# Performance work log

Measured on AMD Instinct MI355X. Metric: run time of the kernel, lower is better.

The kernel has to match this reference:

```python
import jax, jax.numpy as jnp
import numpy as np

N_NODES = 50000
N_EDGES = 800000
F_IN = 128
HID = 256


def setup_inputs() -> dict:
    key = jax.random.key(0)
    ks = jax.random.split(key, 10)
    x = jax.random.normal(ks[0], (N_NODES, F_IN), jnp.float32)
    edge_index = jax.random.randint(ks[1], (2, N_EDGES), 0, N_NODES, jnp.int32)
    # Glorot-ish scaled weights (PyG Linear default init style)
    def w(k, o, i):
        return jax.random.normal(k, (o, i), jnp.float32) * (1.0 / np.sqrt(i))
    return {
        "x": x,
        "edge_index": edge_index,
        "W1l": w(ks[2], HID, F_IN), "b1l": jnp.zeros((HID,), jnp.float32),
        "W1r": w(ks[3], HID, F_IN),
        "W2l": w(ks[4], HID, HID), "b2l": jnp.zeros((HID,), jnp.float32),
        "W2r": w(ks[5], HID, HID),
        "Wh1": w(ks[6], 4, HID), "bh1": jnp.zeros((4,), jnp.float32),
        "Wh2": w(ks[7], 3, HID), "bh2": jnp.zeros((3,), jnp.float32),
    }


def sage_conv(x, edge_index, Wl, bl, Wr):
    # PyG SAGEConv (aggr='mean'): out_i = Wl @ mean_{j in N(i)} x_j + bl + Wr @ x_i
    src, dst = edge_index[0], edge_index[1]
    n = x.shape[0]
    summed = jax.ops.segment_sum(x[src], dst, num_segments=n)        # [N, F]
    cnt = jax.ops.segment_sum(jnp.ones((src.shape[0],), x.dtype), dst, num_segments=n)
    agg = summed / jnp.maximum(cnt, 1.0)[:, None]                    # isolated nodes -> 0
    return agg @ Wl.T + bl + x @ Wr.T


def reference(x, edge_index, W1l, b1l, W1r, W2l, b2l, W2r, Wh1, bh1, Wh2, bh2):
    h = jax.nn.relu(sage_conv(x, edge_index, W1l, b1l, W1r))
    # dropout(p=0.5) is identity in eval mode
    h = sage_conv(h, edge_index, W2l, b2l, W2r)
    out1 = h @ Wh1.T + bh1   # l2_classifier=False branch
    out2 = h @ Wh2.T + bh2
    return (out1, out2, h)
```

## Files before the change

kernel.cpp:

```cpp
#include <hip/hip_runtime.h>
#include <hip/hip_bf16.h>

typedef short bf16x8 __attribute__((ext_vector_type(8)));
typedef float f32x4 __attribute__((ext_vector_type(4)));

__device__ __forceinline__ float bf2f(__hip_bfloat16 v) { return __bfloat162float(v); }
__device__ __forceinline__ float sh2f(short s) {
    union { float f; unsigned u; } c; c.u = ((unsigned)(unsigned short)s) << 16; return c.f;
}
__device__ __forceinline__ short f2sh(float f) {
    __hip_bfloat16 b = __float2bfloat16(f); return *(short*)&b;
}

__device__ __forceinline__ float loadAny(const void* p, size_t i, int isf32) {
    return isf32 ? ((const float*)p)[i] : bf2f(((const __hip_bfloat16*)p)[i]);
}

__global__ void pre_kernel(const void* __restrict__ x,
                           const void* W1l, const void* W1r, const void* W2l, const void* W2r,
                           const void* b1l, const void* b2l, const void* Wh1, const void* Wh2,
                           const void* bh1, const void* bh2,
                           __hip_bfloat16* __restrict__ xn,
                           __hip_bfloat16* __restrict__ W1c, __hip_bfloat16* __restrict__ W2c,
                           __hip_bfloat16* __restrict__ sb,
                           int* __restrict__ deg, int* __restrict__ flag, int N) {
    __shared__ int sflag;
    int tid = threadIdx.x;
    if (tid < 64) {
        const unsigned short* xu = (const unsigned short*)x;
        unsigned short u = xu[tid * 2];
        unsigned e = (u >> 7) & 0xFF;
        bool good = (u == 0) || (e >= 110 && e <= 137);
        unsigned long long m = __ballot(good);
        if (tid == 0) sflag = (__popcll(m) < 32) ? 1 : 0;
    }
    __syncthreads();
    int isf32 = sflag;
    int gid = blockIdx.x * 256 + tid;
    if (gid == 0) *flag = isf32;
    if (gid < N) deg[gid] = 0;

    int n4 = N * 32;
    if (gid < n4) {
        short4 o;
        if (isf32) {
            float4 v = ((const float4*)x)[gid];
            o.x = f2sh(v.x); o.y = f2sh(v.y); o.z = f2sh(v.z); o.w = f2sh(v.w);
        } else {
            o = ((const short4*)x)[gid];
        }
        ((short4*)xn)[gid] = o;
    }

    if (gid < 65536) {
        int n = gid >> 8, k = gid & 255;
        float v = (k < 128) ? loadAny(W1l, n * 128 + k, isf32)
                            : loadAny(W1r, n * 128 + (k - 128), isf32);
        W1c[gid] = __float2bfloat16(v);
        return;
    }
    int u = gid - 65536;
    if (u < 131072) {
        int n = u >> 9, k = u & 511;
        float v = (k < 256) ? loadAny(W2l, n * 256 + k, isf32)
                            : loadAny(W2r, n * 256 + (k - 256), isf32);
        W2c[u] = __float2bfloat16(v);
        return;
    }
    int s = u - 131072;
    float v;
    if      (s < 256)  v = loadAny(b1l, s, isf32);
    else if (s < 512)  v = loadAny(b2l, s - 256, isf32);
    else if (s < 1536) v = loadAny(Wh1, s - 512, isf32);
    else if (s < 2304) v = loadAny(Wh2, s - 1536, isf32);
    else if (s < 2308) v = loadAny(bh1, s - 2304, isf32);
    else if (s < 2311) v = loadAny(bh2, s - 2308, isf32);
    else return;
    sb[s] = __float2bfloat16(v);
}

__global__ void deg_kernel(const int* __restrict__ ei, int E, int* __restrict__ deg,
                           int* __restrict__ rank) {
    int t = blockIdx.x * blockDim.x + threadIdx.x;
    if (t >= E) return;
    rank[t] = atomicAdd(&deg[ei[E + t]], 1);
}

__global__ __launch_bounds__(256) void scanA_kernel(const int* __restrict__ deg,
                                                    int* __restrict__ off,
                                                    int* __restrict__ bsum, int N) {
    __shared__ int ts[256];
    int t = threadIdx.x;
    int base = blockIdx.x * 1024 + t * 4;
    int v0 = (base + 0 < N) ? deg[base + 0] : 0;
    int v1 = (base + 1 < N) ? deg[base + 1] : 0;
    int v2 = (base + 2 < N) ? deg[base + 2] : 0;
    int v3 = (base + 3 < N) ? deg[base + 3] : 0;
    int i0 = v0, i1 = i0 + v1, i2 = i1 + v2, i3 = i2 + v3;
    ts[t] = i3;
    __syncthreads();
    for (int d = 1; d < 256; d <<= 1) {
        int x = (t >= d) ? ts[t - d] : 0;
        __syncthreads();
        ts[t] += x;
        __syncthreads();
    }
    int excl = (t > 0) ? ts[t - 1] : 0;
    if (base + 0 < N) off[base + 1] = excl + i0;
    if (base + 1 < N) off[base + 2] = excl + i1;
    if (base + 2 < N) off[base + 3] = excl + i2;
    if (base + 3 < N) off[base + 4] = excl + i3;
    if (t == 255) bsum[blockIdx.x] = ts[255];
}

__global__ void addC_kernel(int* __restrict__ off, const int* __restrict__ bsum,
                            int N, int nb) {
    __shared__ int ex[64];
    int t = threadIdx.x;
    if (t < 64) {
        int v = (t < nb) ? bsum[t] : 0;
        for (int d = 1; d < 64; d <<= 1) {
            int y = __shfl_up(v, d, 64);
            if (t >= d) v += y;
        }
        ex[t] = v;
    }
    __syncthreads();
    int i = blockIdx.x * 256 + t;
    if (i == 0) off[0] = 0;
    if (i < N) {
        int b = i >> 10;
        int excl = (b > 0) ? ex[b - 1] : 0;
        off[i + 1] += excl;
    }
}

__global__ void fill_kernel(const int* __restrict__ ei, int E,
                            const int* __restrict__ off, const int* __restrict__ rank,
                            unsigned short* __restrict__ srcs) {
    int t = blockIdx.x * blockDim.x + threadIdx.x;
    if (t >= E) return;
    int dst = ei[E + t];
    int pos = off[dst] + rank[t];
    srcs[pos] = (unsigned short)ei[t];
}

__global__ void gather1_kernel(const __hip_bfloat16* __restrict__ x,
                               const int* __restrict__ off,
                               const unsigned short* __restrict__ srcs,
                               __hip_bfloat16* __restrict__ agg, int N) {
    int gid  = blockIdx.x * blockDim.x + threadIdx.x;
    int wid  = gid >> 6;
    int lane = threadIdx.x & 63;
    int node = wid * 4 + (lane >> 4);
    int t    = lane & 15;
    if (node >= N) return;
    int beg = off[node], end = off[node + 1];
    float a[8] = {0.f, 0.f, 0.f, 0.f, 0.f, 0.f, 0.f, 0.f};
    const bf16x8* xb = (const bf16x8*)x;
    int e = beg;
    for (; e + 7 < end; e += 8) {
        bf16x8 v[8];
#pragma unroll
        for (int j = 0; j < 8; j++) v[j] = xb[(size_t)srcs[e + j] * 16 + t];
#pragma unroll
        for (int j = 0; j < 8; j++)
#pragma unroll
            for (int k = 0; k < 8; k++) a[k] += sh2f(v[j][k]);
    }
    for (; e < end; e++) {
        bf16x8 v = xb[(size_t)srcs[e] * 16 + t];
#pragma unroll
        for (int k = 0; k < 8; k++) a[k] += sh2f(v[k]);
    }
    float inv = 1.0f / fmaxf((float)(end - beg), 1.0f);
    bf16x8 o;
#pragma unroll
    for (int k = 0; k < 8; k++) o[k] = f2sh(a[k] * inv);
    ((bf16x8*)agg)[(size_t)node * 16 + t] = o;
}

__global__ void gather2_kernel(const __hip_bfloat16* __restrict__ h,
                               const int* __restrict__ off,
                               const unsigned short* __restrict__ srcs,
                               __hip_bfloat16* __restrict__ agg, int N) {
    int gid  = blockIdx.x * blockDim.x + threadIdx.x;
    int wid  = gid >> 6;
    int lane = threadIdx.x & 63;
    int node = wid * 2 + (lane >> 5);
    int t    = lane & 31;
    if (node >= N) return;
    int beg = off[node], end = off[node + 1];
    float a[8] = {0.f, 0.f, 0.f, 0.f, 0.f, 0.f, 0.f, 0.f};
    const bf16x8* hb = (const bf16x8*)h;
    int e = beg;
    for (; e + 7 < end; e += 8) {
        bf16x8 v[8];
#pragma unroll
        for (int j = 0; j < 8; j++) v[j] = hb[(size_t)srcs[e + j] * 32 + t];
#pragma unroll
        for (int j = 0; j < 8; j++)
#pragma unroll
            for (int k = 0; k < 8; k++) a[k] += sh2f(v[j][k]);
    }
    for (; e < end; e++) {
        bf16x8 v = hb[(size_t)srcs[e] * 32 + t];
#pragma unroll
        for (int k = 0; k < 8; k++) a[k] += sh2f(v[k]);
    }
    float inv = 1.0f / fmaxf((float)(end - beg), 1.0f);
    bf16x8 o;
#pragma unroll
    for (int k = 0; k < 8; k++) o[k] = f2sh(a[k] * inv);
    ((bf16x8*)agg)[(size_t)node * 32 + t] = o;
}

template <int K, int KA, bool RELU, bool TOOUT>
__device__ __forceinline__ void gemm_body(short* wlds,
                                          const __hip_bfloat16* __restrict__ A1,
                                          const __hip_bfloat16* __restrict__ A2, int M,
                                          const __hip_bfloat16* __restrict__ W,
                                          const __hip_bfloat16* __restrict__ bias,
                                          __hip_bfloat16* __restrict__ outb,
                                          void* __restrict__ dout,
                                          const int* __restrict__ flag) {
    constexpr int KB = K - KA;
    constexpr int NCHUNK = K / 64;
    int rowBlks = (M + 63) / 64;
    int b = blockIdx.x;
    int grp = b >> 4, w = b & 15;
    int rowBlk = grp * 8 + (w & 7);
    int half = w >> 3;
    if (rowBlk >= rowBlks) return;
    int tid  = threadIdx.x;
    int wave = tid >> 6, lane = tid & 63, quad = lane >> 4, l15 = lane & 15;
    int R0 = rowBlk * 64;
    int cbase = half * 128;

    int mrow = min(R0 + wave * 16 + l15, M - 1);

    const short* Ws = (const short*)W;

    auto loadW = [&](int p, bf16x8* wreg) {
#pragma unroll
        for (int i = 0; i < 4; i++) {
            int unit = tid + i * 256;
            int ln = unit & 63, nt = (unit >> 6) & 7, kt = unit >> 9;
            int row = cbase + nt * 16 + (ln & 15);
            int kk  = p * 64 + kt * 32 + (ln >> 4) * 8;
            wreg[i] = *(const bf16x8*)(Ws + (size_t)row * K + kk);
        }
    };
    auto storeW = [&](const bf16x8* wreg) {
#pragma unroll
        for (int i = 0; i < 4; i++) {
            int unit = tid + i * 256;
            *(bf16x8*)&wlds[unit * 8] = wreg[i];
        }
    };
    auto loadA = [&](int kglob) {
        const short* ap = (kglob < KA)
            ? (const short*)A1 + (size_t)mrow * KA + kglob + quad * 8
            : (const short*)A2 + (size_t)mrow * KB + (kglob - KA) + quad * 8;
        return *(const bf16x8*)ap;
    };

    f32x4 acc[8];
#pragma unroll
    for (int nt = 0; nt < 8; nt++) acc[nt] = {0.f, 0.f, 0.f, 0.f};

    bf16x8 wreg[4];
    loadW(0, wreg);
    storeW(wreg);
    __syncthreads();
    bf16x8 a0f = loadA(0);
    bf16x8 a1f = loadA(32);

    for (int p = 0; p < NCHUNK; p++) {
        if (p + 1 < NCHUNK) loadW(p + 1, wreg);
#pragma unroll
        for (int kt = 0; kt < 2; kt++) {
            int kg = p * 64 + kt * 32;
            int kg2 = kg + 64;
            if (kg2 > K - 32) kg2 = K - 32;
            bf16x8 a_next = loadA(kg2);
#pragma unroll
            for (int nt = 0; nt < 8; nt++) {
                bf16x8 bfr = *(const bf16x8*)&wlds[((kt * 8 + nt) * 64 + lane) * 8];
                acc[nt] = __builtin_amdgcn_mfma_f32_16x16x32_bf16(a0f, bfr, acc[nt], 0, 0, 0);
            }
            a0f = a1f;
            a1f = a_next;
        }
        if (p + 1 < NCHUNK) {
            __syncthreads();
            storeW(wreg);
            __syncthreads();
        }
    }

    int isf32 = TOOUT ? *flag : 0;
    float* hf = TOOUT ? ((float*)dout + (size_t)M * 7) : nullptr;
    __hip_bfloat16* hb = TOOUT ? ((__hip_bfloat16*)dout + (size_t)M * 7) : outb;

#pragma unroll
    for (int nt = 0; nt < 8; nt++) {
        int col = cbase + nt * 16 + l15;
        float bv = bf2f(bias[col]);
#pragma unroll
        for (int r = 0; r < 4; r++) {
            int row = R0 + wave * 16 + quad * 4 + r;
            if (row < M) {
                float v = acc[nt][r] + bv;
                if (RELU) v = fmaxf(v, 0.f);
                size_t idx = (size_t)row * 256 + col;
                if (TOOUT && isf32) hf[idx] = v;
                else                hb[idx] = __float2bfloat16(v);
            }
        }
    }
}

__global__ __launch_bounds__(256) void gemm1_kernel(const __hip_bfloat16* __restrict__ A1,
                                                    const __hip_bfloat16* __restrict__ A2, int M,
                                                    const __hip_bfloat16* __restrict__ W,
                                                    const __hip_bfloat16* __restrict__ bias,
                                                    __hip_bfloat16* __restrict__ outb,
                                                    const int* __restrict__ flag) {
    __shared__ short wlds[8192];
    gemm_body<256, 128, true, false>(wlds, A1, A2, M, W, bias, outb, nullptr, flag);
}

__global__ __launch_bounds__(256) void gemm2_kernel(const __hip_bfloat16* __restrict__ A1,
                                                    const __hip_bfloat16* __restrict__ A2, int M,
                                                    const __hip_bfloat16* __restrict__ W,
                                                    const __hip_bfloat16* __restrict__ bias,
                                                    void* __restrict__ dout,
                                                    const int* __restrict__ flag) {
    __shared__ short wlds[8192];
    gemm_body<512, 256, false, true>(wlds, A1, A2, M, W, bias, nullptr, dout, flag);
}

__global__ void heads_kernel(const __hip_bfloat16* __restrict__ sb,
                             void* dout, int N, const int* __restrict__ flag) {
    int isf32 = *flag;
    int node = (blockIdx.x * blockDim.x + threadIdx.x) >> 6;
    int lane = threadIdx.x & 63;
    if (node >= N) return;
    float hv0, hv1, hv2, hv3;
    if (isf32) {
        const float4* hp = (const float4*)((const float*)dout + (size_t)N * 7);
        float4 v = hp[(size_t)node * 64 + lane];
        hv0 = v.x; hv1 = v.y; hv2 = v.z; hv3 = v.w;
    } else {
        const __hip_bfloat162* hp = (const __hip_bfloat162*)((const __hip_bfloat16*)dout + (size_t)N * 7);
        __hip_bfloat162 a = hp[(size_t)node * 128 + 2 * lane];
        __hip_bfloat162 b = hp[(size_t)node * 128 + 2 * lane + 1];
        hv0 = bf2f(a.x); hv1 = bf2f(a.y); hv2 = bf2f(b.x); hv3 = bf2f(b.y);
    }
#pragma unroll
    for (int r = 0; r < 7; r++) {
        const __hip_bfloat16* wrow = (r < 4) ? (sb + 512 + r * 256) : (sb + 1536 + (r - 4) * 256);
        const __hip_bfloat162* wr2 = (const __hip_bfloat162*)wrow;
        __hip_bfloat162 wa = wr2[2 * lane];
        __hip_bfloat162 wb = wr2[2 * lane + 1];
        float p = hv0 * bf2f(wa.x) + hv1 * bf2f(wa.y) + hv2 * bf2f(wb.x) + hv3 * bf2f(wb.y);
        for (int off = 32; off > 0; off >>= 1) p += __shfl_down(p, off, 64);
        if (lane == 0) {
            float bias = (r < 4) ? bf2f(sb[2304 + r]) : bf2f(sb[2308 + (r - 4)]);
            float v = p + bias;
            size_t idx = (r < 4) ? ((size_t)node * 4 + r)
                                 : ((size_t)N * 4 + (size_t)node * 3 + (r - 4));
            if (isf32) ((float*)dout)[idx] = v;
            else       ((__hip_bfloat16*)dout)[idx] = __float2bfloat16(v);
        }
    }
}

extern "C" void kernel_launch(void* const* d_in, const int* in_sizes, int n_in,
                              void* d_out, int out_size, void* d_ws, size_t ws_size,
                              hipStream_t stream) {
    const void* x   = d_in[0];
    const int*  ei  = (const int*)d_in[1];
    const void* W1l = d_in[2];
    const void* b1l = d_in[3];
    const void* W1r = d_in[4];
    const void* W2l = d_in[5];
    const void* b2l = d_in[6];
    const void* W2r = d_in[7];
    const void* Wh1 = d_in[8];
    const void* bh1 = d_in[9];
    const void* Wh2 = d_in[10];
    const void* bh2 = d_in[11];

    const int N = in_sizes[0] / 128;
    const int E = in_sizes[1] / 2;
    const int NB = (N + 1023) / 1024;

    char* ws = (char*)d_ws;
    int*            offp   = (int*)(ws + 0);
    int*            deg    = (int*)(ws + 262144);
    int*            bsum   = (int*)(ws + 524288);
    unsigned short* srcs   = (unsigned short*)(ws + 786432);
    __hip_bfloat16* W1c    = (__hip_bfloat16*)(ws + 3986432);
    __hip_bfloat16* W2c    = (__hip_bfloat16*)(ws + 4117504);
    __hip_bfloat16* sb     = (__hip_bfloat16*)(ws + 4379648);
    __hip_bfloat16* xn     = (__hip_bfloat16*)(ws + 4387840);
    __hip_bfloat16* h1     = (__hip_bfloat16*)(ws + 17187840);
    int*            rank   = (int*)(ws + 17187840);
    __hip_bfloat16* agg    = (__hip_bfloat16*)(ws + 42787840);
    int*            flag   = (int*)(ws + 68387840);

    pre_kernel<<<(N * 32 + 255) / 256, 256, 0, stream>>>(
        x, W1l, W1r, W2l, W2r, b1l, b2l, Wh1, Wh2, bh1, bh2,
        xn, W1c, W2c, sb, deg, flag, N);

    deg_kernel<<<(E + 255) / 256, 256, 0, stream>>>(ei, E, deg, rank);
    scanA_kernel<<<NB, 256, 0, stream>>>(deg, offp, bsum, N);
    addC_kernel<<<(N + 255) / 256, 256, 0, stream>>>(offp, bsum, N, NB);
    fill_kernel<<<(E + 255) / 256, 256, 0, stream>>>(ei, E, offp, rank, srcs);

    const int rowBlks = (N + 63) / 64;
    const int gemmGrid = ((rowBlks + 7) / 8) * 16;

    {
        int waves = (N + 3) / 4;
        gather1_kernel<<<(waves * 64 + 255) / 256, 256, 0, stream>>>(xn, offp, srcs, agg, N);
    }
    gemm1_kernel<<<gemmGrid, 256, 0, stream>>>(agg, xn, N, W1c, sb, h1, flag);

    {
        int waves = (N + 1) / 2;
        gather2_kernel<<<(waves * 64 + 255) / 256, 256, 0, stream>>>(h1, offp, srcs, agg, N);
    }
    gemm2_kernel<<<gemmGrid, 256, 0, stream>>>(agg, h1, N, W2c, sb + 256, d_out, flag);

    heads_kernel<<<(N + 3) / 4, 256, 0, stream>>>(sb, d_out, N, flag);
}
```

Baseline: 347.4 us.

## Fuse neighbor mean-gather into GEMM kernels with fragment-ordered weights

The separate gather kernels are removed. Each GEMM block now gathers and averages neighbor features for its 64 rows directly into swizzled LDS, then runs MFMA over the full 256 output columns. Weights are pre-permuted into MFMA fragment order so they can be read straight from global memory instead of being staged through LDS with syncs. This drops the agg round-trip through HBM and two kernel launches. In exchange, the gather's latency-bound loads now share blocks with the GEMM, the weight reads rely on cache reuse, and more accumulator registers are needed.

```diff
diff --git a/kernel.cpp b/kernel.cpp
--- a/kernel.cpp
+++ b/kernel.cpp
@@ -21,7 +21,7 @@
                            const void* b1l, const void* b2l, const void* Wh1, const void* Wh2,
                            const void* bh1, const void* bh2,
                            __hip_bfloat16* __restrict__ xn,
-                           __hip_bfloat16* __restrict__ W1c, __hip_bfloat16* __restrict__ W2c,
+                           __hip_bfloat16* __restrict__ W1f, __hip_bfloat16* __restrict__ W2f,
                            __hip_bfloat16* __restrict__ sb,
                            int* __restrict__ deg, int* __restrict__ flag, int N) {
     __shared__ int sflag;
@@ -56,7 +56,8 @@
         int n = gid >> 8, k = gid & 255;
         float v = (k < 128) ? loadAny(W1l, n * 128 + k, isf32)
                             : loadAny(W1r, n * 128 + (k - 128), isf32);
-        W1c[gid] = __float2bfloat16(v);
+        int idx = ((((k >> 5) * 16 + (n >> 4)) * 64) + ((k >> 3) & 3) * 16 + (n & 15)) * 8 + (k & 7);
+        W1f[idx] = __float2bfloat16(v);
         return;
     }
     int u = gid - 65536;
@@ -64,7 +65,8 @@
         int n = u >> 9, k = u & 511;
         float v = (k < 256) ? loadAny(W2l, n * 256 + k, isf32)
                             : loadAny(W2r, n * 256 + (k - 256), isf32);
-        W2c[u] = __float2bfloat16(v);
+        int idx = ((((k >> 5) * 16 + (n >> 4)) * 64) + ((k >> 3) & 3) * 16 + (n & 15)) * 8 + (k & 7);
+        W2f[idx] = __float2bfloat16(v);
         return;
     }
     int s = u - 131072;
@@ -145,158 +147,90 @@
     srcs[pos] = (unsigned short)ei[t];
 }
 
-__global__ void gather1_kernel(const __hip_bfloat16* __restrict__ x,
-                               const int* __restrict__ off,
-                               const unsigned short* __restrict__ srcs,
-                               __hip_bfloat16* __restrict__ agg, int N) {
-    int gid  = blockIdx.x * blockDim.x + threadIdx.x;
-    int wid  = gid >> 6;
-    int lane = threadIdx.x & 63;
-    int node = wid * 4 + (lane >> 4);
-    int t    = lane & 15;
-    if (node >= N) return;
-    int beg = off[node], end = off[node + 1];
-    float a[8] = {0.f, 0.f, 0.f, 0.f, 0.f, 0.f, 0.f, 0.f};
-    const bf16x8* xb = (const bf16x8*)x;
-    int e = beg;
-    for (; e + 7 < end; e += 8) {
-        bf16x8 v[8];
-#pragma unroll
-        for (int j = 0; j < 8; j++) v[j] = xb[(size_t)srcs[e + j] * 16 + t];
-#pragma unroll
-        for (int j = 0; j < 8; j++)
-#pragma unroll
-            for (int k = 0; k < 8; k++) a[k] += sh2f(v[j][k]);
-    }
-    for (; e < end; e++) {
-        bf16x8 v = xb[(size_t)srcs[e] * 16 + t];
-#pragma unroll
-        for (int k = 0; k < 8; k++) a[k] += sh2f(v[k]);
-    }
-    float inv = 1.0f / fmaxf((float)(end - beg), 1.0f);
-    bf16x8 o;
-#pragma unroll
-    for (int k = 0; k < 8; k++) o[k] = f2sh(a[k] * inv);
-    ((bf16x8*)agg)[(size_t)node * 16 + t] = o;
-}
-
-__global__ void gather2_kernel(const __hip_bfloat16* __restrict__ h,
-                               const int* __restrict__ off,
-                               const unsigned short* __restrict__ srcs,
-                               __hip_bfloat16* __restrict__ agg, int N) {
-    int gid  = blockIdx.x * blockDim.x + threadIdx.x;
-    int wid  = gid >> 6;
-    int lane = threadIdx.x & 63;
-    int node = wid * 2 + (lane >> 5);
-    int t    = lane & 31;
-    if (node >= N) return;
-    int beg = off[node], end = off[node + 1];
-    float a[8] = {0.f, 0.f, 0.f, 0.f, 0.f, 0.f, 0.f, 0.f};
-    const bf16x8* hb = (const bf16x8*)h;
-    int e = beg;
-    for (; e + 7 < end; e += 8) {
-        bf16x8 v[8];
-#pragma unroll
-        for (int j = 0; j < 8; j++) v[j] = hb[(size_t)srcs[e + j] * 32 + t];
-#pragma unroll
-        for (int j = 0; j < 8; j++)
-#pragma unroll
-            for (int k = 0; k < 8; k++) a[k] += sh2f(v[j][k]);
-    }
-    for (; e < end; e++) {
-        bf16x8 v = hb[(size_t)srcs[e] * 32 + t];
-#pragma unroll
-        for (int k = 0; k < 8; k++) a[k] += sh2f(v[k]);
-    }
-    float inv = 1.0f / fmaxf((float)(end - beg), 1.0f);
-    bf16x8 o;
-#pragma unroll
-    for (int k = 0; k < 8; k++) o[k] = f2sh(a[k] * inv);
-    ((bf16x8*)agg)[(size_t)node * 32 + t] = o;
-}
-
 template <int K, int KA, bool RELU, bool TOOUT>
-__device__ __forceinline__ void gemm_body(short* wlds,
-                                          const __hip_bfloat16* __restrict__ A1,
-                                          const __hip_bfloat16* __restrict__ A2, int M,
-                                          const __hip_bfloat16* __restrict__ W,
-                                          const __hip_bfloat16* __restrict__ bias,
-                                          __hip_bfloat16* __restrict__ outb,
-                                          void* __restrict__ dout,
-                                          const int* __restrict__ flag) {
-    constexpr int KB = K - KA;
-    constexpr int NCHUNK = K / 64;
-    int rowBlks = (M + 63) / 64;
-    int b = blockIdx.x;
-    int grp = b >> 4, w = b & 15;
-    int rowBlk = grp * 8 + (w & 7);
-    int half = w >> 3;
-    if (rowBlk >= rowBlks) return;
+__device__ __forceinline__ void gg_body(short* alds,
+                                        const __hip_bfloat16* __restrict__ T, int M,
+                                        const int* __restrict__ off,
+                                        const unsigned short* __restrict__ srcs,
+                                        const short* __restrict__ Wf,
+                                        const __hip_bfloat16* __restrict__ bias,
+                                        __hip_bfloat16* __restrict__ outb,
+                                        void* __restrict__ dout,
+                                        const int* __restrict__ flag) {
+    constexpr int UROW = KA / 8;
+    constexpr int LPN  = UROW;
+    constexpr int NPW  = 64 / LPN;
+    constexpr int ITER = 64 / (4 * NPW);
+    constexpr int KT   = K / 32;
+
     int tid  = threadIdx.x;
     int wave = tid >> 6, lane = tid & 63, quad = lane >> 4, l15 = lane & 15;
-    int R0 = rowBlk * 64;
-    int cbase = half * 128;
-
-    int mrow = min(R0 + wave * 16 + l15, M - 1);
-
-    const short* Ws = (const short*)W;
-
-    auto loadW = [&](int p, bf16x8* wreg) {
-#pragma unroll
-        for (int i = 0; i < 4; i++) {
-            int unit = tid + i * 256;
-            int ln = unit & 63, nt = (unit >> 6) & 7, kt = unit >> 9;
-            int row = cbase + nt * 16 + (ln & 15);
-            int kk  = p * 64 + kt * 32 + (ln >> 4) * 8;
-            wreg[i] = *(const bf16x8*)(Ws + (size_t)row * K + kk);
+    int R0 = blockIdx.x * 64;
+
+    {
+        int t    = lane & (LPN - 1);
+        int nsub = lane / LPN;
+        const bf16x8* tb = (const bf16x8*)T;
+#pragma unroll
+        for (int it = 0; it < ITER; ++it) {
+            int rloc = it * (4 * NPW) + wave * NPW + nsub;
+            int node = R0 + rloc;
+            if (node < M) {
+                int beg = off[node], end = off[node + 1];
+                float a[8] = {0.f, 0.f, 0.f, 0.f, 0.f, 0.f, 0.f, 0.f};
+                int e = beg;
+                for (; e + 7 < end; e += 8) {
+                    bf16x8 v[8];
+#pragma unroll
+                    for (int j = 0; j < 8; j++) v[j] = tb[(size_t)srcs[e + j] * UROW + t];
+#pragma unroll
+                    for (int j = 0; j < 8; j++)
+#pragma unroll
+                        for (int k = 0; k < 8; k++) a[k] += sh2f(v[j][k]);
+                }
+                for (; e < end; e++) {
+                    bf16x8 v = tb[(size_t)srcs[e] * UROW + t];
+#pragma unroll
+                    for (int k = 0; k < 8; k++) a[k] += sh2f(v[k]);
+                }
+                float inv = 1.0f / fmaxf((float)(end - beg), 1.0f);
+                bf16x8 o;
+#pragma unroll
+                for (int k = 0; k < 8; k++) o[k] = f2sh(a[k] * inv);
+                *(bf16x8*)&alds[(rloc * UROW + (t ^ (rloc & 7))) * 8] = o;
+            }
+        }
+    }
+    __syncthreads();
+
+    int rloc_m = wave * 16 + l15;
+    int mrow = min(R0 + rloc_m, M - 1);
+    const short* Ts = (const short*)T;
+
+    auto loadA = [&](int kglob) -> bf16x8 {
+        if (kglob < KA) {
+            int u = (kglob >> 3) + quad;
+            return *(const bf16x8*)&alds[(rloc_m * UROW + (u ^ (rloc_m & 7))) * 8];
+        } else {
+            return *(const bf16x8*)(Ts + (size_t)mrow * KA + (kglob - KA) + quad * 8);
         }
     };
-    auto storeW = [&](const bf16x8* wreg) {
-#pragma unroll
-        for (int i = 0; i < 4; i++) {
-            int unit = tid + i * 256;
-            *(bf16x8*)&wlds[unit * 8] = wreg[i];
-        }
-    };
-    auto loadA = [&](int kglob) {
-        const short* ap = (kglob < KA)
-            ? (const short*)A1 + (size_t)mrow * KA + kglob + quad * 8
-            : (const short*)A2 + (size_t)mrow * KB + (kglob - KA) + quad * 8;
-        return *(const bf16x8*)ap;
-    };
-
-    f32x4 acc[8];
-#pragma unroll
-    for (int nt = 0; nt < 8; nt++) acc[nt] = {0.f, 0.f, 0.f, 0.f};
-
-    bf16x8 wreg[4];
-    loadW(0, wreg);
-    storeW(wreg);
-    __syncthreads();
-    bf16x8 a0f = loadA(0);
-    bf16x8 a1f = loadA(32);
-
-    for (int p = 0; p < NCHUNK; p++) {
-        if (p + 1 < NCHUNK) loadW(p + 1, wreg);
-#pragma unroll
-        for (int kt = 0; kt < 2; kt++) {
-            int kg = p * 64 + kt * 32;
-            int kg2 = kg + 64;
-            if (kg2 > K - 32) kg2 = K - 32;
-            bf16x8 a_next = loadA(kg2);
-#pragma unroll
-            for (int nt = 0; nt < 8; nt++) {
-                bf16x8 bfr = *(const bf16x8*)&wlds[((kt * 8 + nt) * 64 + lane) * 8];
-                acc[nt] = __builtin_amdgcn_mfma_f32_16x16x32_bf16(a0f, bfr, acc[nt], 0, 0, 0);
-            }
-            a0f = a1f;
-            a1f = a_next;
-        }
-        if (p + 1 < NCHUNK) {
-            __syncthreads();
-            storeW(wreg);
-            __syncthreads();
-        }
+
+    f32x4 acc[16];
+#pragma unroll
+    for (int nt = 0; nt < 16; nt++) acc[nt] = {0.f, 0.f, 0.f, 0.f};
+
+    bf16x8 aCur = loadA(0);
+#pragma unroll
+    for (int kt = 0; kt < KT; ++kt) {
+        bf16x8 aNext = aCur;
+        if (kt + 1 < KT) aNext = loadA((kt + 1) * 32);
+#pragma unroll
+        for (int nt = 0; nt < 16; ++nt) {
+            bf16x8 b = *(const bf16x8*)(Wf + (size_t)((kt * 16 + nt) * 64 + lane) * 8);
+            acc[nt] = __builtin_amdgcn_mfma_f32_16x16x32_bf16(aCur, b, acc[nt], 0, 0, 0);
+        }
+        aCur = aNext;
     }
 
     int isf32 = TOOUT ? *flag : 0;
@@ -304,8 +238,8 @@
     __hip_bfloat16* hb = TOOUT ? ((__hip_bfloat16*)dout + (size_t)M * 7) : outb;
 
 #pragma unroll
-    for (int nt = 0; nt < 8; nt++) {
-        int col = cbase + nt * 16 + l15;
+    for (int nt = 0; nt < 16; nt++) {
+        int col = nt * 16 + l15;
         float bv = bf2f(bias[col]);
 #pragma unroll
         for (int r = 0; r < 4; r++) {
@@ -321,24 +255,28 @@
     }
 }
 
-__global__ __launch_bounds__(256) void gemm1_kernel(const __hip_bfloat16* __restrict__ A1,
-                                                    const __hip_bfloat16* __restrict__ A2, int M,
-                                                    const __hip_bfloat16* __restrict__ W,
-                                                    const __hip_bfloat16* __restrict__ bias,
-                                                    __hip_bfloat16* __restrict__ outb,
-                                                    const int* __restrict__ flag) {
-    __shared__ short wlds[8192];
-    gemm_body<256, 128, true, false>(wlds, A1, A2, M, W, bias, outb, nullptr, flag);
-}
-
-__global__ __launch_bounds__(256) void gemm2_kernel(const __hip_bfloat16* __restrict__ A1,
-                                                    const __hip_bfloat16* __restrict__ A2, int M,
-                                                    const __hip_bfloat16* __restrict__ W,
-                                                    const __hip_bfloat16* __restrict__ bias,
-                                                    void* __restrict__ dout,
-                                                    const int* __restrict__ flag) {
-    __shared__ short wlds[8192];
-    gemm_body<512, 256, false, true>(wlds, A1, A2, M, W, bias, nullptr, dout, flag);
+__global__ __launch_bounds__(256, 3) void gemm1_kernel(const __hip_bfloat16* __restrict__ xn,
+                                                       int M,
+                                                       const int* __restrict__ off,
+                                                       const unsigned short* __restrict__ srcs,
+                                                       const short* __restrict__ Wf,
+                                                       const __hip_bfloat16* __restrict__ bias,
+                                                       __hip_bfloat16* __restrict__ outb,
+                                                       const int* __restrict__ flag) {
+    __shared__ short alds[64 * 16 * 8];
+    gg_body<256, 128, true, false>(alds, xn, M, off, srcs, Wf, bias, outb, nullptr, flag);
+}
+
+__global__ __launch_bounds__(256, 3) void gemm2_kernel(const __hip_bfloat16* __restrict__ h1,
+                                                       int M,
+                                                       const int* __restrict__ off,
+                                                       const unsigned short* __restrict__ srcs,
+                                                       const short* __restrict__ Wf,
+                                                       const __hip_bfloat16* __restrict__ bias,
+                                                       void* __restrict__ dout,
+                                                       const int* __restrict__ flag) {
+    __shared__ short alds[64 * 32 * 8];
+    gg_body<512, 256, false, true>(alds, h1, M, off, srcs, Wf, bias, nullptr, dout, flag);
 }
 
 __global__ void heads_kernel(const __hip_bfloat16* __restrict__ sb,
@@ -402,18 +340,17 @@
     int*            deg    = (int*)(ws + 262144);
     int*            bsum   = (int*)(ws + 524288);
     unsigned short* srcs   = (unsigned short*)(ws + 786432);
-    __hip_bfloat16* W1c    = (__hip_bfloat16*)(ws + 3986432);
-    __hip_bfloat16* W2c    = (__hip_bfloat16*)(ws + 4117504);
+    __hip_bfloat16* W1f    = (__hip_bfloat16*)(ws + 3986432);
+    __hip_bfloat16* W2f    = (__hip_bfloat16*)(ws + 4117504);
     __hip_bfloat16* sb     = (__hip_bfloat16*)(ws + 4379648);
     __hip_bfloat16* xn     = (__hip_bfloat16*)(ws + 4387840);
     __hip_bfloat16* h1     = (__hip_bfloat16*)(ws + 17187840);
     int*            rank   = (int*)(ws + 17187840);
-    __hip_bfloat16* agg    = (__hip_bfloat16*)(ws + 42787840);
     int*            flag   = (int*)(ws + 68387840);
 
     pre_kernel<<<(N * 32 + 255) / 256, 256, 0, stream>>>(
         x, W1l, W1r, W2l, W2r, b1l, b2l, Wh1, Wh2, bh1, bh2,
-        xn, W1c, W2c, sb, deg, flag, N);
+        xn, W1f, W2f, sb, deg, flag, N);
 
     deg_kernel<<<(E + 255) / 256, 256, 0, stream>>>(ei, E, deg, rank);
     scanA_kernel<<<NB, 256, 0, stream>>>(deg, offp, bsum, N);
@@ -421,19 +358,10 @@
     fill_kernel<<<(E + 255) / 256, 256, 0, stream>>>(ei, E, offp, rank, srcs);
 
     const int rowBlks = (N + 63) / 64;
-    const int gemmGrid = ((rowBlks + 7) / 8) * 16;
-
-    {
-        int waves = (N + 3) / 4;
-        gather1_kernel<<<(waves * 64 + 255) / 256, 256, 0, stream>>>(xn, offp, srcs, agg, N);
-    }
-    gemm1_kernel<<<gemmGrid, 256, 0, stream>>>(agg, xn, N, W1c, sb, h1, flag);
-
-    {
-        int waves = (N + 1) / 2;
-        gather2_kernel<<<(waves * 64 + 255) / 256, 256, 0, stream>>>(h1, offp, srcs, agg, N);
-    }
-    gemm2_kernel<<<gemmGrid, 256, 0, stream>>>(agg, h1, N, W2c, sb + 256, d_out, flag);
+
+    gemm1_kernel<<<rowBlks, 256, 0, stream>>>(xn, N, offp, srcs, (const short*)W1f, sb, h1, flag);
+
+    gemm2_kernel<<<rowBlks, 256, 0, stream>>>(h1, N, offp, srcs, (const short*)W2f, sb + 256, d_out, flag);
 
     heads_kernel<<<(N + 3) / 4, 256, 0, stream>>>(sb, d_out, N, flag);
 }
```

Result: slower. 361.2 us (+3.9%).
